# Optimization experiments

Measured on AMD Instinct MI355X. Metric: run time of the kernel, lower is better.

## Reference

```python
import jax, jax.numpy as jnp
import numpy as np
from jax.scipy.special import logsumexp

B, S, D, T = 32, 512, 768, 9


def setup_inputs() -> dict:
    key = jax.random.key(0)
    ks = jax.random.split(key, 12)
    s = 0.05
    return {
        "x": jax.random.normal(ks[0], (B, S, D), jnp.float32),
        "tags": jax.random.randint(ks[1], (B, S), 0, T, jnp.int32),
        "mask": jnp.ones((B, S), jnp.bool_),
        "w_ih_f": jax.random.normal(ks[2], (4 * D, D), jnp.float32) * s,
        "w_hh_f": jax.random.normal(ks[3], (4 * D, D), jnp.float32) * s,
        "b_f": jnp.zeros((4 * D,), jnp.float32),
        "w_ih_b": jax.random.normal(ks[4], (4 * D, D), jnp.float32) * s,
        "w_hh_b": jax.random.normal(ks[5], (4 * D, D), jnp.float32) * s,
        "b_b": jnp.zeros((4 * D,), jnp.float32),
        "w_cls": jax.random.normal(ks[6], (T, 2 * D), jnp.float32) * s,
        "b_cls": jnp.zeros((T,), jnp.float32),
        "transitions": jax.random.normal(ks[7], (T, T), jnp.float32) * 0.1,
        "start_trans": jax.random.normal(ks[8], (T,), jnp.float32) * 0.1,
        "end_trans": jax.random.normal(ks[9], (T,), jnp.float32) * 0.1,
    }


def _lstm_dir(x, w_ih, w_hh, b):
    # x: [B,S,D] -> hidden states [B,S,H]; PyTorch gate order i,f,g,o.
    Bb, Ss, _ = x.shape
    H = w_hh.shape[1]
    xg = jnp.einsum('bsd,gd->bsg', x, w_ih) + b  # precompute input projections [B,S,4H]

    def step(carry, xg_t):
        h, c = carry
        g = xg_t + h @ w_hh.T
        i, f, gg, o = jnp.split(g, 4, axis=-1)
        c = jax.nn.sigmoid(f) * c + jax.nn.sigmoid(i) * jnp.tanh(gg)
        h = jax.nn.sigmoid(o) * jnp.tanh(c)
        return (h, c), h

    init = (jnp.zeros((Bb, H), x.dtype), jnp.zeros((Bb, H), x.dtype))
    _, hs = jax.lax.scan(step, init, jnp.swapaxes(xg, 0, 1))  # time-major scan
    return jnp.swapaxes(hs, 0, 1)


def _crf_loss(emissions, tags, mask, transitions, start_trans, end_trans):
    # emissions [B,S,T]; negative token-mean log-likelihood (pytorch-crf).
    mf = mask.astype(emissions.dtype)
    # ---- numerator: score of the gold path (fully vectorized) ----
    em = jnp.take_along_axis(emissions, tags[..., None], axis=-1)[..., 0]  # [B,S]
    tr = transitions[tags[:, :-1], tags[:, 1:]]                            # [B,S-1]
    num = start_trans[tags[:, 0]] + em[:, 0]
    num = num + jnp.sum((tr + em[:, 1:]) * mf[:, 1:], axis=1)
    last_idx = jnp.sum(mask.astype(jnp.int32), axis=1) - 1
    last_tags = jnp.take_along_axis(tags, last_idx[:, None], axis=1)[:, 0]
    num = num + end_trans[last_tags]
    # ---- denominator: forward algorithm via scan over time ----
    score0 = start_trans + emissions[:, 0]  # [B,T]

    def step(score, inp):
        em_t, m_t = inp  # [B,T], [B]
        nxt = logsumexp(score[:, :, None] + transitions[None] + em_t[:, None, :], axis=1)
        return jnp.where(m_t[:, None], nxt, score), None

    em_tm = jnp.swapaxes(emissions[:, 1:], 0, 1)  # [S-1,B,T]
    m_tm = jnp.swapaxes(mask[:, 1:], 0, 1)        # [S-1,B]
    score, _ = jax.lax.scan(step, score0, (em_tm, m_tm))
    den = logsumexp(score + end_trans, axis=1)
    llh = num - den
    return -(jnp.sum(llh) / jnp.sum(mf))  # reduction='token_mean', negated


def reference(x, tags, mask, w_ih_f, w_hh_f, b_f, w_ih_b, w_hh_b, b_b,
              w_cls, b_cls, transitions, start_trans, end_trans):
    h_f = _lstm_dir(x, w_ih_f, w_hh_f, b_f)
    h_b = _lstm_dir(x[:, ::-1], w_ih_b, w_hh_b, b_b)[:, ::-1]
    h = jnp.concatenate([h_f, h_b], axis=-1)          # [B,S,2D]
    emissions = h @ w_cls.T + b_cls                   # [B,S,T]
    return _crf_loss(emissions, tags, mask, transitions, start_trans, end_trans)
```

## Files before the change

### kernel.cpp

```cpp
#include <hip/hip_runtime.h>
#include <stdint.h>

#define BB 32
#define SS 512
#define DD 768
#define GG 3072
#define NTAG 9
#define BSR (BB*SS)
#define EMS 12

typedef __attribute__((ext_vector_type(8))) short bf16x8;
typedef __attribute__((ext_vector_type(4))) float f32x4;

__device__ __forceinline__ float b2f(unsigned short s) {
    union { unsigned u; float f; } v; v.u = ((unsigned)s) << 16; return v.f;
}
__device__ __forceinline__ unsigned short f2b(float f) {
    union { float f; unsigned u; } v; v.f = f;
    unsigned r = v.u + 0x7FFFu + ((v.u >> 16) & 1u);
    return (unsigned short)(r >> 16);
}
__device__ __forceinline__ int pack2(float a, float b) {
    return (int)f2b(a) | ((int)f2b(b) << 16);
}
__device__ __forceinline__ float sigm_(float x) { return 1.f / (1.f + __expf(-x)); }
__device__ __forceinline__ float tanh_(float x) {
    float e = __expf(2.f * x);
    return 1.f - 2.f / (e + 1.f);
}

__global__ void k_diag(float* out, float v) { out[0] = v; }

__global__ void k_permw(const float* __restrict__ src, unsigned short* __restrict__ dst) {
    int gp = blockIdx.x;
    int g = (gp & 3) * DD + (gp >> 2);
    const float* s = src + (size_t)g * DD;
    unsigned short* d = dst + (size_t)gp * DD;
    for (int j = threadIdx.x; j < DD; j += blockDim.x) d[j] = f2b(s[j]);
}
__global__ void k_permb(const float* __restrict__ src, float* __restrict__ dst) {
    int gp = blockIdx.x * blockDim.x + threadIdx.x;
    if (gp < GG) dst[gp] = src[(gp & 3) * DD + (gp >> 2)];
}

#define BM 128
#define BN 128
#define BK 32
__global__ __launch_bounds__(256, 2) void k_gemm_xg(
    const float* __restrict__ X,
    const unsigned short* __restrict__ Wp,
    const float* __restrict__ bias,
    unsigned short* __restrict__ Xg,
    int rev)
{
    __shared__ unsigned short As[BM * BK];
    __shared__ unsigned short Bs[BN * BK];
    int tid = threadIdx.x;
    int lane = tid & 63, w = tid >> 6;
    int wm = w >> 1, wn = w & 1;
    int rowBase = blockIdx.x * BM;
    int colBase = blockIdx.y * BN;

    f32x4 acc[4][4];
#pragma unroll
    for (int mf = 0; mf < 4; ++mf)
#pragma unroll
        for (int nf = 0; nf < 4; ++nf) { acc[mf][nf][0]=0.f; acc[mf][nf][1]=0.f; acc[mf][nf][2]=0.f; acc[mf][nf][3]=0.f; }

    for (int kt = 0; kt < DD / BK; ++kt) {
#pragma unroll
        for (int c = 0; c < 2; ++c) {
            int id = tid * 2 + c;
            int r = id >> 2, ko = id & 3;
            int rowg = rowBase + r;
            int srow;
            if (rev) { int b = rowg >> 9, t = rowg & 511; srow = b * SS + (SS - 1 - t); }
            else srow = rowg;
            const float* src = X + (size_t)srow * DD + kt * BK + ko * 8;
            float4 v0 = *(const float4*)(src);
            float4 v1 = *(const float4*)(src + 4);
            int blk = ko ^ ((r >> 1) & 3);
            *(int4*)(&As[r * BK + blk * 8]) =
                make_int4(pack2(v0.x, v0.y), pack2(v0.z, v0.w), pack2(v1.x, v1.y), pack2(v1.z, v1.w));
        }
#pragma unroll
        for (int c = 0; c < 2; ++c) {
            int id = tid * 2 + c;
            int r = id >> 2, ko = id & 3;
            int4 v = *(const int4*)(Wp + (size_t)(colBase + r) * DD + kt * BK + ko * 8);
            int blk = ko ^ ((r >> 1) & 3);
            *(int4*)(&Bs[r * BK + blk * 8]) = v;
        }
        __syncthreads();
        bf16x8 af[4], bfr[4];
        int ko = lane >> 4;
#pragma unroll
        for (int mf = 0; mf < 4; ++mf) {
            int r = wm * 64 + mf * 16 + (lane & 15);
            af[mf] = *(const bf16x8*)(&As[r * BK + (ko ^ ((r >> 1) & 3)) * 8]);
        }
#pragma unroll
        for (int nf = 0; nf < 4; ++nf) {
            int r = wn * 64 + nf * 16 + (lane & 15);
            bfr[nf] = *(const bf16x8*)(&Bs[r * BK + (ko ^ ((r >> 1) & 3)) * 8]);
        }
#pragma unroll
        for (int mf = 0; mf < 4; ++mf)
#pragma unroll
            for (int nf = 0; nf < 4; ++nf)
                acc[mf][nf] = __builtin_amdgcn_mfma_f32_16x16x32_bf16(af[mf], bfr[nf], acc[mf][nf], 0, 0, 0);
        __syncthreads();
    }
#pragma unroll
    for (int mf = 0; mf < 4; ++mf)
#pragma unroll
        for (int nf = 0; nf < 4; ++nf) {
            int colg = colBase + wn * 64 + nf * 16 + (lane & 15);
            float bv = bias[colg];
#pragma unroll
            for (int i = 0; i < 4; ++i) {
                int rowg = rowBase + wm * 64 + mf * 16 + (lane >> 4) * 4 + i;
                Xg[(size_t)rowg * GG + colg] = f2b(acc[mf][nf][i] + bv);
            }
        }
}

#define NWG 64
#define GR 48
__global__ __launch_bounds__(384, 1) void k_lstm(
    const unsigned short* __restrict__ xg_f, const unsigned short* __restrict__ xg_b,
    const unsigned short* __restrict__ whh_f, const unsigned short* __restrict__ whh_b,
    unsigned short* __restrict__ hs_f, unsigned short* __restrict__ hs_b,
    unsigned int* __restrict__ flags,
    unsigned int* __restrict__ done)
{
    int bid = blockIdx.x;

    if (bid >= 2 * NWG) {
        int dir = bid - 2 * NWG;
        if (threadIdx.x >= 64) return;
        int lane = threadIdx.x;
        const unsigned int* flg = flags + (size_t)dir * SS * 64;
        unsigned int* dn = done + (size_t)dir * SS * 128;
        for (int t = 0; t < SS - 1; ++t) {
            const unsigned long long* fq = (const unsigned long long*)(flg + (size_t)t * 64);
            if (lane < 32) {
                while (__hip_atomic_load(fq + lane, __ATOMIC_RELAXED, __HIP_MEMORY_SCOPE_AGENT)
                       != 0x0000000100000001ULL)
                    __builtin_amdgcn_s_sleep(1);
            }
            if (lane < 4)
                __hip_atomic_store(dn + (size_t)t * 128 + lane * 32, 1u,
                                   __ATOMIC_RELAXED, __HIP_MEMORY_SCOPE_AGENT);
        }
        return;
    }

    int dir = bid >> 6;
    int wg = bid & 63;
    const unsigned short* xg = dir ? xg_b : xg_f;
    const unsigned short* whh = dir ? whh_b : whh_f;
    unsigned short* hs = dir ? hs_b : hs_f;
    unsigned int* flgD = flags + (size_t)dir * SS * 64;
    const unsigned int* dnD = done + (size_t)dir * SS * 128 + (wg & 3) * 32;

    int tid = threadIdx.x;
    int lane = tid & 63, w = tid >> 6;
    int mt = w >> 1, nt = w & 1;
    int g0 = wg * GR;
    int ko = lane >> 4;

    int wrow = g0 + mt * 16 + (lane & 15);
    bf16x8 wf[24];
#pragma unroll
    for (int kt = 0; kt < 24; ++kt)
        wf[kt] = *(const bf16x8*)(whh + (size_t)wrow * DD + kt * 32 + ko * 8);

    int bcol = nt * 16 + (lane & 15);
    int g4 = wg * 12 + mt * 4;
    int gp4 = g0 + mt * 16 + ko * 4;
    const unsigned short* xgrow = xg + (size_t)bcol * SS * GG + gp4;
    unsigned short* hrow = hs + (size_t)bcol * SS * DD;
    float c = 0.f;

    short4 xv = *(const short4*)xgrow;
    for (int t = 0; t < SS; ++t) {
        f32x4 acc;
        acc[0] = b2f((unsigned short)xv.x);
        acc[1] = b2f((unsigned short)xv.y);
        acc[2] = b2f((unsigned short)xv.z);
        acc[3] = b2f((unsigned short)xv.w);
        if (t > 0) {
            const unsigned short* hb = hrow + (size_t)(t - 1) * DD + ko * 8;
#pragma unroll
            for (int kt = 0; kt < 24; ++kt) {
                bf16x8 hv = *(const bf16x8*)(hb + kt * 32);
                acc = __builtin_amdgcn_mfma_f32_16x16x32_bf16(wf[kt], hv, acc, 0, 0, 0);
            }
        }
        float si = sigm_(acc[0]);
        float sf = sigm_(acc[1]);
        float tg = tanh_(acc[2]);
        float so = sigm_(acc[3]);
        c = sf * c + si * tg;
        float h = so * tanh_(c);

        unsigned short hb16 = f2b(h);
        unsigned short pb16 = (unsigned short)__shfl_xor((int)hb16, 16, 64);
        unsigned hp = (unsigned)hb16 | ((unsigned)pb16 << 16);
        unsigned hp2 = (unsigned)__shfl_xor((int)hp, 32, 64);
        if (ko == 0) {
            unsigned long long v8 = ((unsigned long long)hp2 << 32) | (unsigned long long)hp;
            __hip_atomic_store((unsigned long long*)(hrow + (size_t)t * DD + g4), v8,
                               __ATOMIC_RELAXED, __HIP_MEMORY_SCOPE_AGENT);
        }

        if (t == SS - 1) break;

        asm volatile("s_waitcnt vmcnt(0)" ::: "memory");
        __syncthreads();
        if (tid == 0)
            __hip_atomic_store(flgD + (size_t)t * 64 + wg, 1u,
                               __ATOMIC_RELAXED, __HIP_MEMORY_SCOPE_AGENT);

        xv = *(const short4*)(xgrow + (size_t)(t + 1) * GG);

        while (__hip_atomic_load(dnD + (size_t)t * 128, __ATOMIC_RELAXED, __HIP_MEMORY_SCOPE_AGENT) == 0)
            __builtin_amdgcn_s_sleep(1);
        asm volatile("" ::: "memory");
    }
}

__global__ void k_emis(const unsigned short* __restrict__ hs_f, const unsigned short* __restrict__ hs_b,
                       const float* __restrict__ wcls, const float* __restrict__ bcls,
                       float* __restrict__ em)
{
    int row = blockIdx.x * 4 + (threadIdx.x >> 6);
    int lane = threadIdx.x & 63;
    int b = row >> 9, t = row & 511;
    const unsigned long long* hfq = (const unsigned long long*)(hs_f + (size_t)row * DD);
    const unsigned long long* hbq = (const unsigned long long*)(hs_b + ((size_t)(b * SS + (SS - 1 - t))) * DD);
    float p[NTAG];
#pragma unroll
    for (int tau = 0; tau < NTAG; ++tau) p[tau] = 0.f;
#pragma unroll
    for (int it = 0; it < 3; ++it) {
        int j4 = lane + it * 64;
        unsigned long long af = hfq[j4];
        unsigned long long ab = hbq[j4];
#pragma unroll
        for (int e = 0; e < 4; ++e) {
            int j = j4 * 4 + e;
            float hv  = b2f((unsigned short)(af >> (16 * e)));
            float hv2 = b2f((unsigned short)(ab >> (16 * e)));
#pragma unroll
            for (int tau = 0; tau < NTAG; ++tau) {
                p[tau] += hv * wcls[tau * 2 * DD + j];
                p[tau] += hv2 * wcls[tau * 2 * DD + DD + j];
            }
        }
    }
#pragma unroll
    for (int tau = 0; tau < NTAG; ++tau) {
        float v = p[tau];
        for (int m = 32; m; m >>= 1) v += __shfl_xor(v, m, 64);
        if (lane == 0) em[(size_t)row * EMS + tau] = v + bcls[tau];
    }
}

__global__ void k_crf(const float* __restrict__ em, const int* __restrict__ tags,
                      const float* __restrict__ trans, const float* __restrict__ start_t,
                      const float* __restrict__ end_t, float* __restrict__ llh)
{
    int b = blockIdx.x;
    int lane = threadIdx.x;
    const int* tg = tags + b * SS;
    const float* emb = em + (size_t)b * SS * EMS;

    float np = 0.f;
    for (int it = 0; it < 8; ++it) {
        int t = 1 + lane + it * 64;
        if (t < SS) {
            int t0 = tg[t - 1], t1 = tg[t];
            np += trans[t0 * NTAG + t1] + emb[t * EMS + t1];
        }
    }
    for (int m = 32; m; m >>= 1) np += __shfl_xor(np, m, 64);

    float score, ec;
    float tc[NTAG];
    if (lane < NTAG) {
        score = start_t[lane] + emb[lane];
        ec = end_t[lane];
#pragma unroll
        for (int i = 0; i < NTAG; ++i) tc[i] = trans[i * NTAG + lane];
    } else {
        score = -1e30f; ec = 0.f;
#pragma unroll
        for (int i = 0; i < NTAG; ++i) tc[i] = 0.f;
    }
    int eidx = (lane < NTAG) ? lane : 0;
    for (int t = 1; t < SS; ++t) {
        float vv[NTAG];
        float mx = -1e30f;
#pragma unroll
        for (int i = 0; i < NTAG; ++i) {
            float si = __shfl(score, i, 64);
            vv[i] = si + tc[i];
            mx = fmaxf(mx, vv[i]);
        }
        float sum = 0.f;
#pragma unroll
        for (int i = 0; i < NTAG; ++i) sum += __expf(vv[i] - mx);
        float ns = mx + __logf(sum) + emb[t * EMS + eidx];
        score = (lane < NTAG) ? ns : -1e30f;
    }
    float sv = (lane < NTAG) ? score + ec : -1e30f;
    float mx = sv;
    for (int m = 32; m; m >>= 1) mx = fmaxf(mx, __shfl_xor(mx, m, 64));
    float se = (lane < NTAG) ? __expf(sv - mx) : 0.f;
    for (int m = 32; m; m >>= 1) se += __shfl_xor(se, m, 64);
    float den = mx + __logf(se);
    if (lane == 0) {
        float num = np + start_t[tg[0]] + emb[tg[0]] + end_t[tg[SS - 1]];
        llh[b] = num - den;
    }
}

__global__ void k_loss(const float* __restrict__ llh, float* __restrict__ out) {
    int lane = threadIdx.x;
    float v = (lane < BB) ? llh[lane] : 0.f;
    for (int m = 32; m; m >>= 1) v += __shfl_xor(v, m, 64);
    if (lane == 0) out[0] = -v / (float)(BB * SS);
}

extern "C" void kernel_launch(void* const* d_in, const int* in_sizes, int n_in,
                              void* d_out, int out_size, void* d_ws, size_t ws_size,
                              hipStream_t stream) {
    (void)in_sizes; (void)n_in; (void)out_size;
    const float* x      = (const float*)d_in[0];
    const int* tags     = (const int*)d_in[1];
    const float* wihF   = (const float*)d_in[3];
    const float* whhF   = (const float*)d_in[4];
    const float* bF     = (const float*)d_in[5];
    const float* wihB   = (const float*)d_in[6];
    const float* whhB   = (const float*)d_in[7];
    const float* bBi    = (const float*)d_in[8];
    const float* wcls   = (const float*)d_in[9];
    const float* bcls   = (const float*)d_in[10];
    const float* trans  = (const float*)d_in[11];
    const float* startT = (const float*)d_in[12];
    const float* endT   = (const float*)d_in[13];
    float* out = (float*)d_out;

    const size_t szW  = (size_t)GG * DD * 2;
    const size_t szB  = GG * 4;
    const size_t szXg = (size_t)BSR * GG * 2;
    const size_t szHs = (size_t)BB * SS * DD * 2;
    const size_t szEm = (size_t)BSR * EMS * 4;
    const size_t szFl = (size_t)2 * SS * 64 * 4;
    const size_t szDn = (size_t)2 * SS * 128 * 4;
    const size_t NEED = 3*szW + 2*szB + 2*szXg + 2*szHs + szEm + szFl + szDn + 8192;

    if (ws_size < NEED) {
        k_diag<<<1, 1, 0, stream>>>(out, (float)(ws_size >> 20));
        return;
    }

    char* wp = (char*)d_ws;
    auto alloc = [&](size_t bytes) { char* p = wp; wp += (bytes + 255) & ~(size_t)255; return p; };
    unsigned short* whhFp = (unsigned short*)alloc(szW);
    unsigned short* whhBp = (unsigned short*)alloc(szW);
    unsigned short* wihP  = (unsigned short*)alloc(szW);
    float* bFp = (float*)alloc(szB);
    float* bBp = (float*)alloc(szB);
    unsigned short* hsF = (unsigned short*)alloc(szHs);
    unsigned short* hsB = (unsigned short*)alloc(szHs);
    float* em  = (float*)alloc(szEm);
    float* llh = (float*)alloc(256);
    unsigned int* flags = (unsigned int*)alloc(szFl);
    unsigned int* done  = (unsigned int*)alloc(szDn);
    unsigned short* xgF = (unsigned short*)alloc(szXg);
    unsigned short* xgB = (unsigned short*)alloc(szXg);

    k_permw<<<GG, 256, 0, stream>>>(whhF, whhFp);
    k_permw<<<GG, 256, 0, stream>>>(whhB, whhBp);
    k_permb<<<GG / 256, 256, 0, stream>>>(bF, bFp);
    k_permb<<<GG / 256, 256, 0, stream>>>(bBi, bBp);
    hipMemsetAsync(flags, 0, szFl, stream);
    hipMemsetAsync(done, 0, szDn, stream);

    dim3 gg(BSR / BM, GG / BN);
    k_permw<<<GG, 256, 0, stream>>>(wihF, wihP);
    k_gemm_xg<<<gg, 256, 0, stream>>>(x, wihP, bFp, xgF, 0);
    k_permw<<<GG, 256, 0, stream>>>(wihB, wihP);
    k_gemm_xg<<<gg, 256, 0, stream>>>(x, wihP, bBp, xgB, 1);

    k_lstm<<<2 * NWG + 2, 384, 0, stream>>>(xgF, xgB, whhFp, whhBp, hsF, hsB, flags, done);

    k_emis<<<BSR / 4, 256, 0, stream>>>(hsF, hsB, wcls, bcls, em);
    k_crf<<<BB, 64, 0, stream>>>(em, tags, trans, startT, endT, llh);
    k_loss<<<1, 64, 0, stream>>>(llh, out);
}
```

Before: 3.964 ms.

## Replace aggregator-block barrier with direct all-to-all flag polling in LSTM recurrence

Removes the two extra aggregator workgroups that gathered per-workgroup step flags and republished a 'done' flag. Each recurrent workgroup now has its first wave poll all 64 peer flags directly, one per lane, with the flags padded to a 16-byte stride, followed by a block barrier. This drops one hop of global-memory signalling per timestep. In exchange, every workgroup now polls 64 flags, which adds memory traffic and contention on each step.

```diff
diff --git a/kernel.cpp b/kernel.cpp
--- a/kernel.cpp
+++ b/kernel.cpp
@@ -8,6 +8,7 @@
 #define NTAG 9
 #define BSR (BB*SS)
 #define EMS 12
+#define FLS 4
 
 typedef __attribute__((ext_vector_type(8))) short bf16x8;
 typedef __attribute__((ext_vector_type(4))) float f32x4;
@@ -131,38 +132,15 @@
     const unsigned short* __restrict__ xg_f, const unsigned short* __restrict__ xg_b,
     const unsigned short* __restrict__ whh_f, const unsigned short* __restrict__ whh_b,
     unsigned short* __restrict__ hs_f, unsigned short* __restrict__ hs_b,
-    unsigned int* __restrict__ flags,
-    unsigned int* __restrict__ done)
+    unsigned int* __restrict__ flags)
 {
     int bid = blockIdx.x;
-
-    if (bid >= 2 * NWG) {
-        int dir = bid - 2 * NWG;
-        if (threadIdx.x >= 64) return;
-        int lane = threadIdx.x;
-        const unsigned int* flg = flags + (size_t)dir * SS * 64;
-        unsigned int* dn = done + (size_t)dir * SS * 128;
-        for (int t = 0; t < SS - 1; ++t) {
-            const unsigned long long* fq = (const unsigned long long*)(flg + (size_t)t * 64);
-            if (lane < 32) {
-                while (__hip_atomic_load(fq + lane, __ATOMIC_RELAXED, __HIP_MEMORY_SCOPE_AGENT)
-                       != 0x0000000100000001ULL)
-                    __builtin_amdgcn_s_sleep(1);
-            }
-            if (lane < 4)
-                __hip_atomic_store(dn + (size_t)t * 128 + lane * 32, 1u,
-                                   __ATOMIC_RELAXED, __HIP_MEMORY_SCOPE_AGENT);
-        }
-        return;
-    }
-
     int dir = bid >> 6;
     int wg = bid & 63;
     const unsigned short* xg = dir ? xg_b : xg_f;
     const unsigned short* whh = dir ? whh_b : whh_f;
     unsigned short* hs = dir ? hs_b : hs_f;
-    unsigned int* flgD = flags + (size_t)dir * SS * 64;
-    const unsigned int* dnD = done + (size_t)dir * SS * 128 + (wg & 3) * 32;
+    unsigned int* flgD = flags + (size_t)dir * SS * 64 * FLS;
 
     int tid = threadIdx.x;
     int lane = tid & 63, w = tid >> 6;
@@ -220,13 +198,17 @@
         asm volatile("s_waitcnt vmcnt(0)" ::: "memory");
         __syncthreads();
         if (tid == 0)
-            __hip_atomic_store(flgD + (size_t)t * 64 + wg, 1u,
+            __hip_atomic_store(flgD + (size_t)t * 64 * FLS + wg * FLS, 1u,
                                __ATOMIC_RELAXED, __HIP_MEMORY_SCOPE_AGENT);
 
         xv = *(const short4*)(xgrow + (size_t)(t + 1) * GG);
 
-        while (__hip_atomic_load(dnD + (size_t)t * 128, __ATOMIC_RELAXED, __HIP_MEMORY_SCOPE_AGENT) == 0)
-            __builtin_amdgcn_s_sleep(1);
+        if (w == 0) {
+            const unsigned int* fp = flgD + (size_t)t * 64 * FLS + lane * FLS;
+            while (__hip_atomic_load(fp, __ATOMIC_RELAXED, __HIP_MEMORY_SCOPE_AGENT) == 0)
+                __builtin_amdgcn_s_sleep(1);
+        }
+        __syncthreads();
         asm volatile("" ::: "memory");
     }
 }
@@ -358,9 +340,8 @@
     const size_t szXg = (size_t)BSR * GG * 2;
     const size_t szHs = (size_t)BB * SS * DD * 2;
     const size_t szEm = (size_t)BSR * EMS * 4;
-    const size_t szFl = (size_t)2 * SS * 64 * 4;
-    const size_t szDn = (size_t)2 * SS * 128 * 4;
-    const size_t NEED = 3*szW + 2*szB + 2*szXg + 2*szHs + szEm + szFl + szDn + 8192;
+    const size_t szFl = (size_t)2 * SS * 64 * FLS * 4;
+    const size_t NEED = 3*szW + 2*szB + 2*szXg + 2*szHs + szEm + szFl + 8192;
 
     if (ws_size < NEED) {
         k_diag<<<1, 1, 0, stream>>>(out, (float)(ws_size >> 20));
@@ -379,7 +360,6 @@
     float* em  = (float*)alloc(szEm);
     float* llh = (float*)alloc(256);
     unsigned int* flags = (unsigned int*)alloc(szFl);
-    unsigned int* done  = (unsigned int*)alloc(szDn);
     unsigned short* xgF = (unsigned short*)alloc(szXg);
     unsigned short* xgB = (unsigned short*)alloc(szXg);
 
@@ -388,7 +368,6 @@
     k_permb<<<GG / 256, 256, 0, stream>>>(bF, bFp);
     k_permb<<<GG / 256, 256, 0, stream>>>(bBi, bBp);
     hipMemsetAsync(flags, 0, szFl, stream);
-    hipMemsetAsync(done, 0, szDn, stream);
 
     dim3 gg(BSR / BM, GG / BN);
     k_permw<<<GG, 256, 0, stream>>>(wihF, wihP);
@@ -396,7 +375,7 @@
     k_permw<<<GG, 256, 0, stream>>>(wihB, wihP);
     k_gemm_xg<<<gg, 256, 0, stream>>>(x, wihP, bBp, xgB, 1);
 
-    k_lstm<<<2 * NWG + 2, 384, 0, stream>>>(xgF, xgB, whhFp, whhBp, hsF, hsB, flags, done);
+    k_lstm<<<2 * NWG, 384, 0, stream>>>(xgF, xgB, whhFp, whhBp, hsF, hsB, flags);
 
     k_emis<<<BSR / 4, 256, 0, stream>>>(hsF, hsB, wcls, bcls, em);
     k_crf<<<BB, 64, 0, stream>>>(em, tags, trans, startT, endT, llh);
```

After: 4.016 ms. Within noise of the previous version (+1.3%).
